# Performance work log

Measured on AMD Instinct MI355X. Metric: run time of the kernel, lower is better.

The kernel has to match this reference:

```python
import jax, jax.numpy as jnp
import numpy as np

UNITS = 512
GROUPS = 32
EPS = 1e-3  # keras GroupNormalization default epsilon


def group_norm(x, gamma, beta):
    # x: [B,H,W,C]; normalize over (H,W, channels-within-group)
    B, H, W, C = x.shape
    xg = x.reshape(B, H, W, GROUPS, C // GROUPS)
    mean = xg.mean(axis=(1, 2, 4), keepdims=True)
    var = xg.var(axis=(1, 2, 4), keepdims=True)
    xn = (xg - mean) * jax.lax.rsqrt(var + EPS)
    return xn.reshape(B, H, W, C) * gamma + beta


def setup_inputs() -> dict:
    key = jax.random.key(0)
    ks = jax.random.split(key, 6)
    B, H, W, C = 16, 32, 32, UNITS
    std = 0.02  # RandomNormal(stddev=0.02) kernel init
    return {
        "x": jax.random.normal(ks[0], (B, H, W, C), jnp.float32),
        "gamma": jnp.ones((C,), jnp.float32),
        "beta": jnp.zeros((C,), jnp.float32),
        "Wq": std * jax.random.normal(ks[1], (C, UNITS), jnp.float32),
        "bq": jnp.zeros((UNITS,), jnp.float32),
        "Wk": std * jax.random.normal(ks[2], (C, UNITS), jnp.float32),
        "bk": jnp.zeros((UNITS,), jnp.float32),
        "Wv": std * jax.random.normal(ks[3], (C, UNITS), jnp.float32),
        "bv": jnp.zeros((UNITS,), jnp.float32),
        "Wp": std * jax.random.normal(ks[4], (UNITS, UNITS), jnp.float32),
        "bp": jnp.zeros((UNITS,), jnp.float32),
    }


def reference(x, gamma, beta, Wq, bq, Wk, bk, Wv, bv, Wp, bp):
    B, H, W, C = x.shape
    scale = jnp.float32(UNITS) ** -0.5
    xn = group_norm(x, gamma, beta)  # note: original residual uses normalized input
    # flatten spatial dims to N = H*W tokens (same math as bhwc/bHWc einsums)
    xf = xn.reshape(B, H * W, C)
    q = xf @ Wq + bq
    k = xf @ Wk + bk
    v = xf @ Wv + bv
    scores = jnp.einsum('bnc,bmc->bnm', q, k) * scale  # [B, N, N]
    attn = jax.nn.softmax(scores, axis=-1)
    out = jnp.einsum('bnm,bmc->bnc', attn, v)
    proj = out @ Wp + bp
    return xn + proj.reshape(B, H, W, C)
```

## Files before the change

kernel.cpp:

```cpp
#include <hip/hip_runtime.h>
#include <math.h>

#define BATCH 16
#define NTOK  1024
#define CH    512
#define NGRP  32
#define GSZ   16
#define EPSV  1e-3f
#define MTOT  (BATCH*NTOK)
#define SCALE 0.04419417382415922f
#define SEXP  (SCALE*1.4426950408889634f)

typedef unsigned short u16;
typedef __attribute__((ext_vector_type(4))) float f32x4;
typedef __attribute__((ext_vector_type(8))) short s16x8;

__device__ __forceinline__ u16 f2bf(float f) {
    union { float f; unsigned u; } x{f};
    unsigned r = x.u + 0x7fff + ((x.u >> 16) & 1);
    return (u16)(r >> 16);
}

__device__ __forceinline__ void gld16(const u16* g, u16* l) {
    __builtin_amdgcn_global_load_lds(
        (const __attribute__((address_space(1))) void*)g,
        (__attribute__((address_space(3))) void*)l, 16, 0, 0);
}

__global__ __launch_bounds__(256) void gn_stats(const float* __restrict__ x,
                                                float2* __restrict__ stats) {
    int bg = blockIdx.x;
    int b = bg >> 5, g = bg & 31;
    const float* base = x + (size_t)b * NTOK * CH + g * GSZ;
    float s = 0.f, ss = 0.f;
    for (int i = threadIdx.x; i < 4096; i += 256) {
        int p = i >> 2, c4 = i & 3;
        float4 v = *(const float4*)(base + (size_t)p * CH + c4 * 4);
        s  += v.x + v.y + v.z + v.w;
        ss += v.x * v.x + v.y * v.y + v.z * v.z + v.w * v.w;
    }
    for (int off = 32; off; off >>= 1) {
        s  += __shfl_down(s, off);
        ss += __shfl_down(ss, off);
    }
    __shared__ float2 part[4];
    if ((threadIdx.x & 63) == 0) part[threadIdx.x >> 6] = make_float2(s, ss);
    __syncthreads();
    if (threadIdx.x == 0) {
        float S = 0.f, SS = 0.f;
        for (int i = 0; i < 4; i++) { S += part[i].x; SS += part[i].y; }
        float mean = S * (1.f / 16384.f);
        float var  = SS * (1.f / 16384.f) - mean * mean;
        stats[bg] = make_float2(mean, rsqrtf(var + EPSV));
    }
}

__global__ __launch_bounds__(256) void gn_apply(const float* __restrict__ x,
                                                const float2* __restrict__ stats,
                                                const float* __restrict__ gamma,
                                                const float* __restrict__ beta,
                                                float* __restrict__ xn,
                                                u16* __restrict__ xnb) {
    size_t total = (size_t)MTOT * CH / 4;
    for (size_t i4 = (size_t)blockIdx.x * 256 + threadIdx.x; i4 < total;
         i4 += (size_t)gridDim.x * 256) {
        size_t flat = i4 * 4;
        int c = (int)(flat & (CH - 1));
        int b = (int)(flat >> 19);
        int g = c >> 4;
        float2 st = stats[(b << 5) + g];
        float4 xv = *(const float4*)(x + flat);
        float4 gv = *(const float4*)(gamma + c);
        float4 bv = *(const float4*)(beta + c);
        float4 o;
        o.x = (xv.x - st.x) * st.y * gv.x + bv.x;
        o.y = (xv.y - st.x) * st.y * gv.y + bv.y;
        o.z = (xv.z - st.x) * st.y * gv.z + bv.z;
        o.w = (xv.w - st.x) * st.y * gv.w + bv.w;
        *(float4*)(xn + flat) = o;
        uint2 h;
        h.x = (unsigned)f2bf(o.x) | ((unsigned)f2bf(o.y) << 16);
        h.y = (unsigned)f2bf(o.z) | ((unsigned)f2bf(o.w) << 16);
        *(uint2*)(xnb + flat) = h;
    }
}

__global__ __launch_bounds__(256) void weights_prep(
    const float* __restrict__ Wq, const float* __restrict__ Wk,
    const float* __restrict__ Wv, const float* __restrict__ Wp,
    u16* __restrict__ WTqkv, u16* __restrict__ WTp) {
    int z = blockIdx.z;
    const float* src = z == 0 ? Wq : z == 1 ? Wk : z == 2 ? Wv : Wp;
    u16* dst = z < 3 ? WTqkv + (size_t)z * CH * CH : WTp;
    __shared__ u16 tile[64][66];
    int r0 = blockIdx.y * 64, c0 = blockIdx.x * 64;
    int t = threadIdx.x;
    for (int i = 0; i < 16; i++) {
        int idx = i * 256 + t;
        int r = idx >> 6, c = idx & 63;
        tile[r][c] = f2bf(src[(size_t)(r0 + r) * CH + c0 + c]);
    }
    __syncthreads();
    for (int i = 0; i < 16; i++) {
        int idx = i * 256 + t;
        int oc = idx >> 6, orr = idx & 63;
        dst[(size_t)(c0 + oc) * CH + r0 + orr] = tile[orr][oc];
    }
}

__global__ void prep_bias(const float* __restrict__ bq, const float* __restrict__ bk,
                          const float* __restrict__ bv, float* __restrict__ bqkv) {
    int t = blockIdx.x * 256 + threadIdx.x;
    bqkv[t] = t < 512 ? bq[t] : (t < 1024 ? bk[t - 512] : bv[t - 1024]);
}

__global__ __launch_bounds__(256) void vt_transpose(const u16* __restrict__ in,
                                                    u16* __restrict__ out,
                                                    int R, int C, int ldIn,
                                                    long sIn, long sOut) {
    __shared__ u16 tile[64][66];
    int z = blockIdx.z;
    in  += (size_t)z * sIn;
    out += (size_t)z * sOut;
    int r0 = blockIdx.y * 64, c0 = blockIdx.x * 64;
    int t = threadIdx.x;
    for (int i = 0; i < 16; i++) {
        int idx = i * 256 + t;
        int r = idx >> 6, c = idx & 63;
        tile[r][c] = in[(size_t)(r0 + r) * ldIn + c0 + c];
    }
    __syncthreads();
    for (int i = 0; i < 16; i++) {
        int idx = i * 256 + t;
        int oc = idx >> 6, orr = idx & 63;
        out[(size_t)(c0 + oc) * R + r0 + orr] = tile[orr][oc];
    }
}

template <bool BIAS, bool RES, bool OUTF32>
__global__ __launch_bounds__(256) void gemm_bt(
    const u16* __restrict__ A, const u16* __restrict__ B, void* __restrict__ Cout,
    const float* __restrict__ bias, const float* __restrict__ res,
    int K, int lda, int ldb, int ldc,
    long sA, long sB, long sC, float alpha) {
    __shared__ __align__(16) u16 Asm[8192];
    __shared__ __align__(16) u16 Bsm[8192];

    unsigned flat = blockIdx.x + gridDim.x * (blockIdx.y + gridDim.y * blockIdx.z);
    unsigned nb = gridDim.x * gridDim.y * gridDim.z;
    unsigned lf = (flat & 7) * (nb >> 3) + (flat >> 3);
    unsigned pb = gridDim.x * gridDim.y;
    unsigned bz = lf / pb, rem = lf - bz * pb;
    unsigned by = rem / gridDim.x, bx = rem - by * gridDim.x;

    A += (size_t)bz * sA;
    B += (size_t)bz * sB;
    size_t zc = (size_t)bz * sC;

    int t = threadIdx.x;
    int wave = t >> 6, lane = t & 63;
    int wm = wave >> 1, wn = wave & 1;
    int rowA0 = by * 128;
    int colB0 = bx * 128;

    int c16log = (lane & 3) ^ ((lane >> 3) & 3);
    const u16* aG[2]; const u16* bG[2]; u16* aL[2]; u16* bL[2];
#pragma unroll
    for (int j = 0; j < 2; j++) {
        int s = wave * 2 + j;
        int row = s * 16 + (lane >> 2);
        aL[j] = Asm + s * 512;
        bL[j] = Bsm + s * 512;
        aG[j] = A + (size_t)(rowA0 + row) * lda + c16log * 8;
        bG[j] = B + (size_t)(colB0 + row) * ldb + c16log * 8;
    }

    int kg = lane >> 4;
    int aoff[4], boff[4];
#pragma unroll
    for (int i = 0; i < 4; i++) {
        int ra = wm * 64 + i * 16 + (lane & 15);
        aoff[i] = ra * 32 + (kg ^ ((ra >> 1) & 3)) * 8;
        int rb = wn * 64 + i * 16 + (lane & 15);
        boff[i] = rb * 32 + (kg ^ ((rb >> 1) & 3)) * 8;
    }

#define STG_G(buf, ktE)                          \
    {                                            \
        gld16(aG[0] + (ktE), aL[0] + (buf) * 4096); \
        gld16(aG[1] + (ktE), aL[1] + (buf) * 4096); \
        gld16(bG[0] + (ktE), bL[0] + (buf) * 4096); \
        gld16(bG[1] + (ktE), bL[1] + (buf) * 4096); \
    }

    f32x4 acc[4][4] = {};
    int nk = K >> 5;
    STG_G(0, 0);
    __syncthreads();
    for (int kt = 0; kt < nk; kt++) {
        if (kt + 1 < nk) STG_G((kt + 1) & 1, (kt + 1) * 32);
        const u16* as = Asm + (kt & 1) * 4096;
        const u16* bs = Bsm + (kt & 1) * 4096;
        s16x8 af[4], bfr[4];
#pragma unroll
        for (int i = 0; i < 4; i++) {
            af[i]  = *(const s16x8*)(as + aoff[i]);
            bfr[i] = *(const s16x8*)(bs + boff[i]);
        }
#pragma unroll
        for (int mi = 0; mi < 4; mi++)
#pragma unroll
            for (int nj = 0; nj < 4; nj++)
                acc[mi][nj] = __builtin_amdgcn_mfma_f32_16x16x32_bf16(
                    af[mi], bfr[nj], acc[mi][nj], 0, 0, 0);
        __syncthreads();
    }
#undef STG_G

    int r0 = rowA0 + wm * 64 + (lane >> 4) * 4;
    int c0c = colB0 + wn * 64 + (lane & 15);
#pragma unroll
    for (int mi = 0; mi < 4; mi++) {
#pragma unroll
        for (int nj = 0; nj < 4; nj++) {
            int c = c0c + nj * 16;
            float bv = BIAS ? bias[c] : 0.f;
            f32x4 v = acc[mi][nj];
#pragma unroll
            for (int j = 0; j < 4; j++) {
                int rr = r0 + mi * 16 + j;
                float val = v[j] * alpha + bv;
                if (RES) val += res[(size_t)rr * ldc + c];
                if (OUTF32) ((float*)Cout)[zc + (size_t)rr * ldc + c] = val;
                else        ((u16*)Cout)[zc + (size_t)rr * ldc + c] = f2bf(val);
            }
        }
    }
}

__global__ __launch_bounds__(512, 2) void attn_fused(const u16* __restrict__ qkv,
                                                     u16* __restrict__ P) {
    __shared__ __align__(16) u16 Bsm[65536];

    unsigned flat = blockIdx.x;
    unsigned lf = (flat & 7) * 32 + (flat >> 3);
    int b = lf >> 4, mt = lf & 15;

    int t = threadIdx.x, w = t >> 6, lane = t & 63;
    int wr = w >> 1, wn = w & 1;
    int l15 = lane & 15, kg = lane >> 4;

    const u16* qbase = qkv + ((size_t)b * NTOK + mt * 64) * (3 * CH);
    const u16* kbase = qkv + (size_t)b * NTOK * (3 * CH) + CH;

    const u16* qrow = qbase + (size_t)(wr * 16 + l15) * (3 * CH) + kg * 8;
    s16x8 aq[16];
#pragma unroll
    for (int kt = 0; kt < 16; kt++) aq[kt] = *(const s16x8*)(qrow + kt * 32);

    int c16log = (lane & 3) ^ ((lane >> 3) & 3);
    const u16* bG[8];
#pragma unroll
    for (int j = 0; j < 8; j++) {
        int row = (w * 8 + j) * 16 + (lane >> 2);
        bG[j] = kbase + (size_t)row * (3 * CH) + c16log * 8;
    }
    int rb0 = wn * 512 + l15;
    int boff = rb0 * 32 + (kg ^ ((rb0 >> 1) & 3)) * 8;

    f32x4 acc[32];
#pragma unroll
    for (int i = 0; i < 32; i++) acc[i] = f32x4{0.f, 0.f, 0.f, 0.f};

#define STG(buf, kt)                                                        \
    {                                                                       \
        _Pragma("unroll")                                                   \
        for (int j = 0; j < 8; j++)                                         \
            gld16(bG[j] + (kt) * 32, Bsm + (buf) * 32768 + (w * 8 + j) * 512); \
    }

    STG(0, 0);
    __syncthreads();
#pragma unroll
    for (int kt = 0; kt < 16; kt++) {
        if (kt < 15) STG((kt + 1) & 1, kt + 1);
        const u16* bb = Bsm + (kt & 1) * 32768;
#pragma unroll
        for (int nj = 0; nj < 32; nj++) {
            s16x8 bf = *(const s16x8*)(bb + boff + nj * 512);
            acc[nj] = __builtin_amdgcn_mfma_f32_16x16x32_bf16(aq[kt], bf, acc[nj], 0, 0, 0);
        }
        __syncthreads();
    }
#undef STG

    float* redm = (float*)Bsm;
    float* reds = (float*)(Bsm + 256);

    float mrow[4], inv[4], srow[4];
#pragma unroll
    for (int j = 0; j < 4; j++) {
        float m = acc[0][j];
#pragma unroll
        for (int nj = 1; nj < 32; nj++) m = fmaxf(m, acc[nj][j]);
        for (int off = 1; off < 16; off <<= 1) m = fmaxf(m, __shfl_xor(m, off));
        mrow[j] = m;
    }
    if (l15 == 0) {
#pragma unroll
        for (int j = 0; j < 4; j++) redm[(wr * 16 + kg * 4 + j) * 2 + wn] = mrow[j];
    }
    __syncthreads();
#pragma unroll
    for (int j = 0; j < 4; j++) {
        int row = wr * 16 + kg * 4 + j;
        mrow[j] = fmaxf(redm[row * 2], redm[row * 2 + 1]);
    }
#pragma unroll
    for (int j = 0; j < 4; j++) {
        float s = 0.f;
#pragma unroll
        for (int nj = 0; nj < 32; nj++) {
            float e = exp2f((acc[nj][j] - mrow[j]) * SEXP);
            acc[nj][j] = e;
            s += e;
        }
        for (int off = 1; off < 16; off <<= 1) s += __shfl_xor(s, off);
        srow[j] = s;
    }
    if (l15 == 0) {
#pragma unroll
        for (int j = 0; j < 4; j++) reds[(wr * 16 + kg * 4 + j) * 2 + wn] = srow[j];
    }
    __syncthreads();
#pragma unroll
    for (int j = 0; j < 4; j++) {
        int row = wr * 16 + kg * 4 + j;
        inv[j] = 1.f / (reds[row * 2] + reds[row * 2 + 1]);
    }

    size_t pbase = (size_t)b * NTOK * NTOK + (size_t)mt * 64 * NTOK;
#pragma unroll
    for (int h = 0; h < 2; h++) {
        __syncthreads();
        if (wn == h) {
#pragma unroll
            for (int nj = 0; nj < 32; nj++) {
                int c = nj * 16 + l15;
                int c16 = c >> 3, cw = c & 7;
#pragma unroll
                for (int j = 0; j < 4; j++) {
                    int row = wr * 16 + kg * 4 + j;
                    int pc16 = c16 ^ ((row >> 2) & 7);
                    Bsm[row * 512 + pc16 * 8 + cw] = f2bf(acc[nj][j] * inv[j]);
                }
            }
        }
        __syncthreads();
#pragma unroll
        for (int i = 0; i < 8; i++) {
            int flat16 = (i * 512 + t) * 8;
            int row = flat16 >> 9, c = flat16 & 511;
            int pc16 = (c >> 3) ^ ((row >> 2) & 7);
            uint4 vv = *(const uint4*)(Bsm + row * 512 + pc16 * 8);
            *(uint4*)(P + pbase + (size_t)row * NTOK + h * 512 + c) = vv;
        }
    }
}

extern "C" void kernel_launch(void* const* d_in, const int* in_sizes, int n_in,
                              void* d_out, int out_size, void* d_ws, size_t ws_size,
                              hipStream_t stream) {
    const float* x     = (const float*)d_in[0];
    const float* gamma = (const float*)d_in[1];
    const float* beta  = (const float*)d_in[2];
    const float* Wq    = (const float*)d_in[3];
    const float* bq    = (const float*)d_in[4];
    const float* Wk    = (const float*)d_in[5];
    const float* bk    = (const float*)d_in[6];
    const float* Wv    = (const float*)d_in[7];
    const float* bv    = (const float*)d_in[8];
    const float* Wp    = (const float*)d_in[9];
    const float* bp    = (const float*)d_in[10];
    float* out = (float*)d_out;

    const size_t SZ  = (size_t)MTOT * CH;
    const size_t NSZ = (size_t)NTOK * CH;
    const size_t SCB = (size_t)NTOK * NTOK;

    char* p = (char*)d_ws;
    float*  xn    = (float*)p;   p += SZ * 4;
    u16*    xnb   = (u16*)p;     p += SZ * 2;
    u16*    qkvb  = (u16*)p;     p += (size_t)MTOT * 3 * CH * 2;
    u16*    vt    = (u16*)p;     p += SZ * 2;
    u16*    ao    = (u16*)p;     p += SZ * 2;
    u16*    P     = (u16*)p;     p += (size_t)BATCH * SCB * 2;
    u16*    WTqkv = (u16*)p;     p += (size_t)3 * CH * CH * 2;
    u16*    WTp   = (u16*)p;     p += (size_t)CH * CH * 2;
    float*  bqkv  = (float*)p;   p += 3 * CH * 4;
    float2* stats = (float2*)p;

    dim3 blk(256);

    gn_stats<<<BATCH * NGRP, blk, 0, stream>>>(x, stats);
    gn_apply<<<2048, blk, 0, stream>>>(x, stats, gamma, beta, xn, xnb);
    weights_prep<<<dim3(8, 8, 4), blk, 0, stream>>>(Wq, Wk, Wv, Wp, WTqkv, WTp);
    prep_bias<<<6, blk, 0, stream>>>(bq, bk, bv, bqkv);

    gemm_bt<true, false, false><<<dim3(12, 128, 1), blk, 0, stream>>>(
        xnb, WTqkv, qkvb, bqkv, nullptr, CH, CH, CH, 3 * CH, 0, 0, 0, 1.f);

    vt_transpose<<<dim3(8, 16, BATCH), blk, 0, stream>>>(
        qkvb + 2 * CH, vt, NTOK, CH, 3 * CH, (long)NTOK * 3 * CH, (long)NSZ);

    attn_fused<<<256, 512, 0, stream>>>(qkvb, P);

    gemm_bt<false, false, false><<<dim3(4, 8, BATCH), blk, 0, stream>>>(
        P, vt, ao, nullptr, nullptr, NTOK, NTOK, NTOK, CH,
        (long)SCB, (long)NSZ, (long)NSZ, 1.f);

    gemm_bt<true, true, true><<<dim3(4, 128, 1), blk, 0, stream>>>(
        ao, WTp, out, bp, xn, CH, CH, CH, CH, 0, 0, 0, 1.f);
}
```

Before: 262.2 us.

## Fuse P·V matmul into attention kernel, eliminating the materialized probability matrix

The attention kernel now computes softmax probabilities and immediately multiplies them by V from shared memory, writing the attention output directly instead of storing the full bf16 P matrix and running a separate batched GEMM. The warp layout changes from 4x2 to 2x4 with each warp holding two 16-row groups, and Q fragments are streamed per k-step instead of preloaded. This removes a 32 MB round trip and one launch, but each block now also streams V and runs only 256 blocks, and the launch-bounds minimum-blocks hint was dropped, which may affect occupancy.

```diff
diff --git a/kernel.cpp b/kernel.cpp
--- a/kernel.cpp
+++ b/kernel.cpp
@@ -26,6 +26,8 @@
         (const __attribute__((address_space(1))) void*)g,
         (__attribute__((address_space(3))) void*)l, 16, 0, 0);
 }
+
+#define MFMA16 __builtin_amdgcn_mfma_f32_16x16x32_bf16
 
 __global__ __launch_bounds__(256) void gn_stats(const float* __restrict__ x,
                                                 float2* __restrict__ stats) {
@@ -211,8 +213,7 @@
         for (int mi = 0; mi < 4; mi++)
 #pragma unroll
             for (int nj = 0; nj < 4; nj++)
-                acc[mi][nj] = __builtin_amdgcn_mfma_f32_16x16x32_bf16(
-                    af[mi], bfr[nj], acc[mi][nj], 0, 0, 0);
+                acc[mi][nj] = MFMA16(af[mi], bfr[nj], acc[mi][nj], 0, 0, 0);
         __syncthreads();
     }
 #undef STG_G
@@ -238,133 +239,205 @@
     }
 }
 
-__global__ __launch_bounds__(512, 2) void attn_fused(const u16* __restrict__ qkv,
-                                                     u16* __restrict__ P) {
-    __shared__ __align__(16) u16 Bsm[65536];
+__global__ __launch_bounds__(512) void attn_fused(const u16* __restrict__ qkv,
+                                                  const u16* __restrict__ vtg,
+                                                  u16* __restrict__ ao) {
+    __shared__ __align__(16) u16 S[65536];
 
     unsigned flat = blockIdx.x;
     unsigned lf = (flat & 7) * 32 + (flat >> 3);
     int b = lf >> 4, mt = lf & 15;
 
     int t = threadIdx.x, w = t >> 6, lane = t & 63;
-    int wr = w >> 1, wn = w & 1;
+    int rt = w >> 2, ct = w & 3;
     int l15 = lane & 15, kg = lane >> 4;
 
-    const u16* qbase = qkv + ((size_t)b * NTOK + mt * 64) * (3 * CH);
-    const u16* kbase = qkv + (size_t)b * NTOK * (3 * CH) + CH;
-
-    const u16* qrow = qbase + (size_t)(wr * 16 + l15) * (3 * CH) + kg * 8;
-    s16x8 aq[16];
-#pragma unroll
-    for (int kt = 0; kt < 16; kt++) aq[kt] = *(const s16x8*)(qrow + kt * 32);
-
+    const u16* kbase = qkv + (size_t)b * NTOK * 1536 + CH;
     int c16log = (lane & 3) ^ ((lane >> 3) & 3);
+
     const u16* bG[8];
 #pragma unroll
     for (int j = 0; j < 8; j++) {
         int row = (w * 8 + j) * 16 + (lane >> 2);
-        bG[j] = kbase + (size_t)row * (3 * CH) + c16log * 8;
-    }
-    int rb0 = wn * 512 + l15;
-    int boff = rb0 * 32 + (kg ^ ((rb0 >> 1) & 3)) * 8;
-
-    f32x4 acc[32];
-#pragma unroll
-    for (int i = 0; i < 32; i++) acc[i] = f32x4{0.f, 0.f, 0.f, 0.f};
-
-#define STG(buf, kt)                                                        \
-    {                                                                       \
-        _Pragma("unroll")                                                   \
-        for (int j = 0; j < 8; j++)                                         \
-            gld16(bG[j] + (kt) * 32, Bsm + (buf) * 32768 + (w * 8 + j) * 512); \
-    }
-
-    STG(0, 0);
+        bG[j] = kbase + (size_t)row * 1536 + c16log * 8;
+    }
+    const u16* qp[2];
+#pragma unroll
+    for (int rg = 0; rg < 2; rg++)
+        qp[rg] = qkv + (size_t)(b * NTOK + mt * 64 + rt * 32 + rg * 16 + l15) * 1536 + kg * 8;
+
+    int rbb = ct * 256 + l15;
+    int boffb = rbb * 32 + ((kg ^ ((rbb >> 1) & 3)) << 3);
+
+    f32x4 acc1[2][16];
+#pragma unroll
+    for (int rg = 0; rg < 2; rg++)
+#pragma unroll
+        for (int nj = 0; nj < 16; nj++) acc1[rg][nj] = f32x4{0.f, 0.f, 0.f, 0.f};
+
+#define KSTG(buf, kt)                                                        \
+    { _Pragma("unroll")                                                      \
+      for (int j = 0; j < 8; j++)                                            \
+          gld16(bG[j] + (kt) * 32, S + (buf) * 32768 + (w * 8 + j) * 512); }
+
+    KSTG(0, 0);
+    s16x8 aqc[2], aqn[2];
+    aqc[0] = *(const s16x8*)(qp[0]);
+    aqc[1] = *(const s16x8*)(qp[1]);
     __syncthreads();
 #pragma unroll
     for (int kt = 0; kt < 16; kt++) {
-        if (kt < 15) STG((kt + 1) & 1, kt + 1);
-        const u16* bb = Bsm + (kt & 1) * 32768;
-#pragma unroll
-        for (int nj = 0; nj < 32; nj++) {
-            s16x8 bf = *(const s16x8*)(bb + boff + nj * 512);
-            acc[nj] = __builtin_amdgcn_mfma_f32_16x16x32_bf16(aq[kt], bf, acc[nj], 0, 0, 0);
-        }
+        if (kt < 15) {
+            KSTG((kt + 1) & 1, kt + 1);
+            aqn[0] = *(const s16x8*)(qp[0] + (kt + 1) * 32);
+            aqn[1] = *(const s16x8*)(qp[1] + (kt + 1) * 32);
+        }
+        const u16* bb = S + (kt & 1) * 32768;
+#pragma unroll
+        for (int nj = 0; nj < 16; nj++) {
+            s16x8 bf = *(const s16x8*)(bb + boffb + nj * 512);
+            acc1[0][nj] = MFMA16(aqc[0], bf, acc1[0][nj], 0, 0, 0);
+            acc1[1][nj] = MFMA16(aqc[1], bf, acc1[1][nj], 0, 0, 0);
+        }
+        if (kt < 15) { aqc[0] = aqn[0]; aqc[1] = aqn[1]; }
         __syncthreads();
     }
-#undef STG
-
-    float* redm = (float*)Bsm;
-    float* reds = (float*)(Bsm + 256);
-
-    float mrow[4], inv[4], srow[4];
-#pragma unroll
-    for (int j = 0; j < 4; j++) {
-        float m = acc[0][j];
-#pragma unroll
-        for (int nj = 1; nj < 32; nj++) m = fmaxf(m, acc[nj][j]);
-        for (int off = 1; off < 16; off <<= 1) m = fmaxf(m, __shfl_xor(m, off));
-        mrow[j] = m;
-    }
+#undef KSTG
+
+    float* redm = (float*)S;
+    float* reds = redm + 256;
+    float mr[2][4], iv[2][4];
+#pragma unroll
+    for (int rg = 0; rg < 2; rg++)
+#pragma unroll
+        for (int j = 0; j < 4; j++) {
+            float m = acc1[rg][0][j];
+#pragma unroll
+            for (int nj = 1; nj < 16; nj++) m = fmaxf(m, acc1[rg][nj][j]);
+            for (int off = 1; off < 16; off <<= 1) m = fmaxf(m, __shfl_xor(m, off));
+            mr[rg][j] = m;
+        }
     if (l15 == 0) {
 #pragma unroll
-        for (int j = 0; j < 4; j++) redm[(wr * 16 + kg * 4 + j) * 2 + wn] = mrow[j];
-    }
-    __syncthreads();
-#pragma unroll
-    for (int j = 0; j < 4; j++) {
-        int row = wr * 16 + kg * 4 + j;
-        mrow[j] = fmaxf(redm[row * 2], redm[row * 2 + 1]);
-    }
-#pragma unroll
-    for (int j = 0; j < 4; j++) {
-        float s = 0.f;
-#pragma unroll
-        for (int nj = 0; nj < 32; nj++) {
-            float e = exp2f((acc[nj][j] - mrow[j]) * SEXP);
-            acc[nj][j] = e;
-            s += e;
-        }
-        for (int off = 1; off < 16; off <<= 1) s += __shfl_xor(s, off);
-        srow[j] = s;
-    }
-    if (l15 == 0) {
-#pragma unroll
-        for (int j = 0; j < 4; j++) reds[(wr * 16 + kg * 4 + j) * 2 + wn] = srow[j];
-    }
-    __syncthreads();
-#pragma unroll
-    for (int j = 0; j < 4; j++) {
-        int row = wr * 16 + kg * 4 + j;
-        inv[j] = 1.f / (reds[row * 2] + reds[row * 2 + 1]);
-    }
-
-    size_t pbase = (size_t)b * NTOK * NTOK + (size_t)mt * 64 * NTOK;
-#pragma unroll
-    for (int h = 0; h < 2; h++) {
+        for (int rg = 0; rg < 2; rg++)
+#pragma unroll
+            for (int j = 0; j < 4; j++)
+                redm[(rt * 32 + rg * 16 + kg * 4 + j) * 4 + ct] = mr[rg][j];
+    }
+    __syncthreads();
+#pragma unroll
+    for (int rg = 0; rg < 2; rg++)
+#pragma unroll
+        for (int j = 0; j < 4; j++) {
+            int row = rt * 32 + rg * 16 + kg * 4 + j;
+            mr[rg][j] = fmaxf(fmaxf(redm[row * 4], redm[row * 4 + 1]),
+                              fmaxf(redm[row * 4 + 2], redm[row * 4 + 3]));
+        }
+#pragma unroll
+    for (int rg = 0; rg < 2; rg++)
+#pragma unroll
+        for (int j = 0; j < 4; j++) {
+            float s = 0.f;
+#pragma unroll
+            for (int nj = 0; nj < 16; nj++) {
+                float e = exp2f((acc1[rg][nj][j] - mr[rg][j]) * SEXP);
+                acc1[rg][nj][j] = e;
+                s += e;
+            }
+            for (int off = 1; off < 16; off <<= 1) s += __shfl_xor(s, off);
+            if (l15 == 0) reds[(rt * 32 + rg * 16 + kg * 4 + j) * 4 + ct] = s;
+        }
+    __syncthreads();
+#pragma unroll
+    for (int rg = 0; rg < 2; rg++)
+#pragma unroll
+        for (int j = 0; j < 4; j++) {
+            int row = rt * 32 + rg * 16 + kg * 4 + j;
+            iv[rg][j] = 1.f / (reds[row * 4] + reds[row * 4 + 1] +
+                               reds[row * 4 + 2] + reds[row * 4 + 3]);
+        }
+    __syncthreads();
+
+    const u16* vG[4];
+#pragma unroll
+    for (int sj = 0; sj < 4; sj++) {
+        int chrow = (w * 4 + sj) * 16 + (lane >> 2);
+        vG[sj] = vtg + ((size_t)b * 512 + chrow) * 1024 + c16log * 8;
+    }
+#define VSTG(buf, hf, c)                                                     \
+    { _Pragma("unroll")                                                      \
+      for (int sj = 0; sj < 4; sj++)                                         \
+          gld16(vG[sj] + (hf) * 512 + (c) * 32,                              \
+                S + 32768 + (buf) * 16384 + (w * 4 + sj) * 512); }
+
+    f32x4 acc2[2][8];
+#pragma unroll
+    for (int rg = 0; rg < 2; rg++)
+#pragma unroll
+        for (int cj = 0; cj < 8; cj++) acc2[rg][cj] = f32x4{0.f, 0.f, 0.f, 0.f};
+
+    int prow[2] = {rt * 32 + l15, rt * 32 + 16 + l15};
+    int chl = ct * 128 + l15;
+    int voffb = chl * 32 + ((kg ^ ((chl >> 1) & 3)) << 3);
+
+    for (int hf = 0; hf < 2; hf++) {
+        VSTG(0, hf, 0);
+        if ((ct >> 1) == hf) {
+            int kb16 = (ct & 1) * 256;
+#pragma unroll
+            for (int rg = 0; rg < 2; rg++)
+#pragma unroll
+                for (int nj = 0; nj < 16; nj++) {
+                    int klocal = kb16 + nj * 16 + l15;
+                    int g = klocal >> 3, ko = klocal & 7;
+#pragma unroll
+                    for (int j = 0; j < 4; j++) {
+                        int row = rt * 32 + rg * 16 + kg * 4 + j;
+                        S[row * 512 + (((g ^ (row & 7))) << 3) + ko] =
+                            f2bf(acc1[rg][nj][j] * iv[rg][j]);
+                    }
+                }
+        }
         __syncthreads();
-        if (wn == h) {
-#pragma unroll
-            for (int nj = 0; nj < 32; nj++) {
-                int c = nj * 16 + l15;
-                int c16 = c >> 3, cw = c & 7;
-#pragma unroll
-                for (int j = 0; j < 4; j++) {
-                    int row = wr * 16 + kg * 4 + j;
-                    int pc16 = c16 ^ ((row >> 2) & 7);
-                    Bsm[row * 512 + pc16 * 8 + cw] = f2bf(acc[nj][j] * inv[j]);
-                }
+        for (int c = 0; c < 16; c++) {
+            if (c < 15) VSTG((c + 1) & 1, hf, c + 1);
+            const u16* vb = S + 32768 + (c & 1) * 16384;
+            s16x8 pa[2];
+#pragma unroll
+            for (int rg = 0; rg < 2; rg++) {
+                int row = prow[rg];
+                pa[rg] = *(const s16x8*)(S + row * 512 + (((c * 4 + kg) ^ (row & 7)) << 3));
             }
-        }
-        __syncthreads();
-#pragma unroll
-        for (int i = 0; i < 8; i++) {
-            int flat16 = (i * 512 + t) * 8;
-            int row = flat16 >> 9, c = flat16 & 511;
-            int pc16 = (c >> 3) ^ ((row >> 2) & 7);
-            uint4 vv = *(const uint4*)(Bsm + row * 512 + pc16 * 8);
-            *(uint4*)(P + pbase + (size_t)row * NTOK + h * 512 + c) = vv;
-        }
+#pragma unroll
+            for (int cj = 0; cj < 8; cj++) {
+                s16x8 vf = *(const s16x8*)(vb + voffb + cj * 512);
+                acc2[0][cj] = MFMA16(pa[0], vf, acc2[0][cj], 0, 0, 0);
+                acc2[1][cj] = MFMA16(pa[1], vf, acc2[1][cj], 0, 0, 0);
+            }
+            __syncthreads();
+        }
+    }
+#undef VSTG
+
+#pragma unroll
+    for (int rg = 0; rg < 2; rg++)
+#pragma unroll
+        for (int cj = 0; cj < 8; cj++)
+#pragma unroll
+            for (int j = 0; j < 4; j++) {
+                int row = rt * 32 + rg * 16 + kg * 4 + j;
+                int ch = ct * 128 + cj * 16 + l15;
+                S[row * 512 + ((((ch >> 3) ^ (row & 7))) << 3) + (ch & 7)] =
+                    f2bf(acc2[rg][cj][j]);
+            }
+    __syncthreads();
+    u16* aop = ao + (size_t)(b * NTOK + mt * 64) * 512;
+#pragma unroll
+    for (int i = 0; i < 8; i++) {
+        int f = i * 512 + t;
+        int row = f >> 6, g = f & 63;
+        uint4 v = *(const uint4*)(S + row * 512 + g * 8);
+        *(uint4*)(aop + (size_t)row * 512 + ((g ^ (row & 7)) << 3)) = v;
     }
 }
 
@@ -386,7 +459,6 @@
 
     const size_t SZ  = (size_t)MTOT * CH;
     const size_t NSZ = (size_t)NTOK * CH;
-    const size_t SCB = (size_t)NTOK * NTOK;
 
     char* p = (char*)d_ws;
     float*  xn    = (float*)p;   p += SZ * 4;
@@ -394,7 +466,6 @@
     u16*    qkvb  = (u16*)p;     p += (size_t)MTOT * 3 * CH * 2;
     u16*    vt    = (u16*)p;     p += SZ * 2;
     u16*    ao    = (u16*)p;     p += SZ * 2;
-    u16*    P     = (u16*)p;     p += (size_t)BATCH * SCB * 2;
     u16*    WTqkv = (u16*)p;     p += (size_t)3 * CH * CH * 2;
     u16*    WTp   = (u16*)p;     p += (size_t)CH * CH * 2;
     float*  bqkv  = (float*)p;   p += 3 * CH * 4;
@@ -413,11 +484,7 @@
     vt_transpose<<<dim3(8, 16, BATCH), blk, 0, stream>>>(
         qkvb + 2 * CH, vt, NTOK, CH, 3 * CH, (long)NTOK * 3 * CH, (long)NSZ);
 
-    attn_fused<<<256, 512, 0, stream>>>(qkvb, P);
-
-    gemm_bt<false, false, false><<<dim3(4, 8, BATCH), blk, 0, stream>>>(
-        P, vt, ao, nullptr, nullptr, NTOK, NTOK, NTOK, CH,
-        (long)SCB, (long)NSZ, (long)NSZ, 1.f);
+    attn_fused<<<256, 512, 0, stream>>>(qkvb, vt, ao);
 
     gemm_bt<true, true, true><<<dim3(4, 128, 1), blk, 0, stream>>>(
         ao, WTp, out, bp, xn, CH, CH, CH, CH, 0, 0, 0, 1.f);
```

Result: slower. 307.8 us (+17.4%).
